# Kernel tuning notes

Hardware: AMD Instinct MI355X
Metric: run time of the kernel (lower is better)

Reference implementation:

```python
import jax, jax.numpy as jnp
import numpy as np

B, T, C = 16, 2048, 68
HEAD = 64

def setup_inputs() -> dict:
    key = jax.random.key(0)
    k1, k2, k3, k4 = jax.random.split(key, 4)
    x = jax.random.normal(k1, (B, T, C), dtype=jnp.float32)
    # Linear(n_embd, head_size, bias=False): y = x @ W, W stored as [C, HEAD]
    Wk = jax.random.normal(k2, (C, HEAD), dtype=jnp.float32) / np.sqrt(C)
    Wq = jax.random.normal(k3, (C, HEAD), dtype=jnp.float32) / np.sqrt(C)
    Wv = jax.random.normal(k4, (C, HEAD), dtype=jnp.float32) / np.sqrt(C)
    return {"x": x, "Wk": Wk, "Wq": Wq, "Wv": Wv}

def reference(x, Wk, Wq, Wv):
    # single-head attention, no causal mask, dropout p=0.0 (identity)
    k = jnp.einsum('btc,ch->bth', x, Wk)   # [B,T,H]
    q = jnp.einsum('btc,ch->bth', x, Wq)   # [B,T,H]
    v = jnp.einsum('btc,ch->bth', x, Wv)   # [B,T,H]
    scale = 1.0 / jnp.sqrt(jnp.asarray(k.shape[-1], k.dtype))
    wei = jnp.einsum('bqh,bkh->bqk', q, k) * scale  # [B,T,T]
    wei = jax.nn.softmax(wei, axis=-1)
    out = jnp.einsum('bqk,bkh->bqh', wei, v)        # [B,T,H]
    return out
```

## Files before the change

kernel.cpp:

```cpp
#include <hip/hip_runtime.h>
#include <hip/hip_bf16.h>

#define BB 16
#define TT 2048
#define CC 68
#define HH 64
#define PP 40

typedef short short8 __attribute__((ext_vector_type(8)));
typedef float floatx4 __attribute__((ext_vector_type(4)));

static __device__ __forceinline__ unsigned short f2bf(float f) {
    union { float f; unsigned u; } v; v.f = f;
    unsigned r = v.u + 0x7fffu + ((v.u >> 16) & 1u);
    return (unsigned short)(r >> 16);
}
static __device__ __forceinline__ unsigned pk2(float a, float b) {
    unsigned ua = __builtin_bit_cast(unsigned, a) + 0x8000u;
    unsigned ub = __builtin_bit_cast(unsigned, b) + 0x8000u;
    return (ua >> 16) | (ub & 0xffff0000u);
}

#define GLD16(gsrc, ldsbase)                                                        \
    __builtin_amdgcn_global_load_lds(                                               \
        (const __attribute__((address_space(1))) unsigned int*)(gsrc),              \
        (__attribute__((address_space(3))) unsigned int*)(ldsbase), 16, 0, 0)

#define WAITV8 asm volatile("s_waitcnt vmcnt(8)" ::: "memory")
#define WAITV0 asm volatile("s_waitcnt vmcnt(0)" ::: "memory")
#define MEMFENCE asm volatile("" ::: "memory")

__global__ __launch_bounds__(256) void prep_w(
        const float* __restrict__ Wk, const float* __restrict__ Wq,
        const float* __restrict__ Wv, unsigned short* __restrict__ Wt) {
    int idx = blockIdx.x * 256 + threadIdx.x;
    if (idx >= 192 * 96) return;
    int n = idx / 96, c = idx - n * 96;
    float v = 0.f;
    if (c < CC) {
        if (n < 64)       v = Wk[c * 64 + n];
        else if (n < 128) v = Wq[c * 64 + (n - 64)] * 0.18033688011112042f;
        else              v = Wv[c * 64 + (n - 128)];
    }
    Wt[idx] = f2bf(v);
}

__global__ __launch_bounds__(256) void qkv_kernel(
        const float* __restrict__ x, const unsigned short* __restrict__ Wt,
        unsigned short* __restrict__ Qb, unsigned short* __restrict__ Kb,
        unsigned short* __restrict__ Vt) {
    int tid = threadIdx.x;
    int wave = tid >> 6, lane = tid & 63, quad = lane >> 4, l15 = lane & 15;
    size_t row0 = (size_t)blockIdx.x * 64;
    int b = (int)(row0 >> 11), t0 = (int)(row0 & 2047);
    size_t myrow = row0 + wave * 16 + l15;
    const float* xr = x + myrow * CC;

    short8 a[3];
    union { short8 s8; unsigned u[4]; } t;
    #pragma unroll
    for (int cs = 0; cs < 2; ++cs) {
        float4 f0 = *(const float4*)(xr + cs * 32 + quad * 8);
        float4 f1 = *(const float4*)(xr + cs * 32 + quad * 8 + 4);
        t.u[0] = pk2(f0.x, f0.y); t.u[1] = pk2(f0.z, f0.w);
        t.u[2] = pk2(f1.x, f1.y); t.u[3] = pk2(f1.z, f1.w);
        a[cs] = t.s8;
    }
    {
        t.u[0] = 0; t.u[1] = 0; t.u[2] = 0; t.u[3] = 0;
        if (quad == 0) {
            float4 f = *(const float4*)(xr + 64);
            t.u[0] = pk2(f.x, f.y); t.u[1] = pk2(f.z, f.w);
        }
        a[2] = t.s8;
    }

    auto loadW = [&](short8 (&w)[3], int nt) {
        #pragma unroll
        for (int cs = 0; cs < 3; ++cs)
            w[cs] = *(const short8*)&Wt[(nt * 16 + l15) * 96 + cs * 32 + quad * 8];
    };

    short8 wf[2][3];
    loadW(wf[0], 0);
    for (int nt = 0; nt < 12; ++nt) {
        if (nt + 1 < 12) loadW(wf[(nt + 1) & 1], nt + 1);
        floatx4 acc = (floatx4){0.f, 0.f, 0.f, 0.f};
        #pragma unroll
        for (int cs = 0; cs < 3; ++cs)
            acc = __builtin_amdgcn_mfma_f32_16x16x32_bf16(a[cs], wf[nt & 1][cs], acc, 0, 0, 0);

        if (nt < 8) {
            unsigned short* dst = (nt < 4) ? Kb : Qb;
            int h = (nt & 3) * 16 + l15;
            #pragma unroll
            for (int r = 0; r < 4; ++r)
                dst[(row0 + wave * 16 + quad * 4 + r) * 64 + h] = f2bf(acc[r]);
        } else {
            int h = (nt - 8) * 16 + l15;
            int tt = t0 + wave * 16 + quad * 4;
            uint2 v2; v2.x = pk2(acc[0], acc[1]); v2.y = pk2(acc[2], acc[3]);
            *(uint2*)&Vt[((size_t)(b * 64 + h)) * TT + tt] = v2;
        }
    }
}

__global__ __launch_bounds__(256) void attn_kernel(
        const unsigned short* __restrict__ Qb,
        const unsigned short* __restrict__ Kb,
        const unsigned short* __restrict__ Vt,
        float* __restrict__ out) {
    __shared__ union {
        unsigned char stg[4][2][8192];
        float accL[64][66];
    } u;
    __shared__ unsigned short Ps[4][32 * PP];
    __shared__ float lL[2][64];

    int tid = threadIdx.x;
    int wave = tid >> 6, lane = tid & 63, quad = lane >> 4, l15 = lane & 15;
    int half = wave >> 1, qh = wave & 1;
    int id = blockIdx.x;
    int b = id & 15, qblk = id >> 4;
    int q0 = qblk * 64 + qh * 32;
    int kbase = half * 1024;
    unsigned short* ps = Ps[wave];

    short8 qf[2][2];
    #pragma unroll
    for (int qs = 0; qs < 2; ++qs)
        #pragma unroll
        for (int kh = 0; kh < 2; ++kh)
            qf[qs][kh] = *(const short8*)&Qb[((size_t)(b * TT + q0 + qs * 16 + l15)) * 64
                                             + kh * 32 + quad * 8];

    floatx4 acc[2][4];
    float lpart[2] = {0.f, 0.f};
    #pragma unroll
    for (int qs = 0; qs < 2; ++qs)
        #pragma unroll
        for (int hb = 0; hb < 4; ++hb) acc[qs][hb] = (floatx4){0.f, 0.f, 0.f, 0.f};

    auto stage = [&](int it, int p) {
        unsigned char* base = u.stg[wave][p];
        int kt = kbase + it * 32;
        #pragma unroll
        for (int i = 0; i < 4; ++i) {
            int ci = i * 64 + lane;
            int kv = ci >> 3, cp = ci & 7, c = cp ^ (kv & 7);
            GLD16(Kb + ((size_t)(b * TT + kt + kv) * 64 + c * 8), base + i * 1024);
        }
        #pragma unroll
        for (int i = 0; i < 4; ++i) {
            int ci = i * 64 + lane;
            int h = ci >> 2, cp = ci & 3, c = cp ^ ((h >> 1) & 3);
            GLD16(Vt + ((size_t)(b * 64 + h) * TT + kt + c * 8), base + 4096 + i * 1024);
        }
    };

    auto compute = [&](int p) {
        const unsigned char* Kbuf = u.stg[wave][p];
        const unsigned char* Vbuf = Kbuf + 4096;

        short8 kf[2][2], vf[4];
        #pragma unroll
        for (int ks = 0; ks < 2; ++ks)
            #pragma unroll
            for (int kh = 0; kh < 2; ++kh) {
                int cp = (kh * 4 + quad) ^ (l15 & 7);
                kf[ks][kh] = *(const short8*)(Kbuf + (ks * 16 + l15) * 128 + cp * 16);
            }
        #pragma unroll
        for (int hb = 0; hb < 4; ++hb) {
            int cp = quad ^ ((l15 >> 1) & 3);
            vf[hb] = *(const short8*)(Vbuf + (hb * 16 + l15) * 64 + cp * 16);
        }

        floatx4 s[2][2];
        #pragma unroll
        for (int qs = 0; qs < 2; ++qs)
            #pragma unroll
            for (int ks = 0; ks < 2; ++ks) {
                floatx4 z = (floatx4){0.f, 0.f, 0.f, 0.f};
                z = __builtin_amdgcn_mfma_f32_16x16x32_bf16(kf[ks][0], qf[qs][0], z, 0, 0, 0);
                z = __builtin_amdgcn_mfma_f32_16x16x32_bf16(kf[ks][1], qf[qs][1], z, 0, 0, 0);
                s[qs][ks] = z;
            }

        #pragma unroll
        for (int qs = 0; qs < 2; ++qs) {
            float lp = 0.f;
            #pragma unroll
            for (int ks = 0; ks < 2; ++ks) {
                float e0 = __builtin_amdgcn_exp2f(s[qs][ks][0]);
                float e1 = __builtin_amdgcn_exp2f(s[qs][ks][1]);
                float e2 = __builtin_amdgcn_exp2f(s[qs][ks][2]);
                float e3 = __builtin_amdgcn_exp2f(s[qs][ks][3]);
                lp += (e0 + e1) + (e2 + e3);
                uint2 w; w.x = pk2(e0, e1); w.y = pk2(e2, e3);
                *(uint2*)&ps[(qs * 16 + l15) * PP + ks * 16 + quad * 4] = w;
            }
            lpart[qs] += lp;
        }

        short8 pf[2];
        #pragma unroll
        for (int qs = 0; qs < 2; ++qs)
            pf[qs] = *(const short8*)&ps[(qs * 16 + l15) * PP + quad * 8];
        #pragma unroll
        for (int qs = 0; qs < 2; ++qs)
            #pragma unroll
            for (int hb = 0; hb < 4; ++hb)
                acc[qs][hb] = __builtin_amdgcn_mfma_f32_16x16x32_bf16(pf[qs], vf[hb], acc[qs][hb], 0, 0, 0);
    };

    stage(0, 0);
    stage(1, 1);
    for (int it = 0; it < 31; ++it) {
        WAITV8;
        compute(it & 1);
        if (it + 2 < 32) { MEMFENCE; stage(it + 2, it & 1); }
    }
    WAITV0;
    compute(1);

    #pragma unroll
    for (int qs = 0; qs < 2; ++qs) {
        float v = lpart[qs];
        v += __shfl_xor(v, 16);
        v += __shfl_xor(v, 32);
        lpart[qs] = v;
    }
    if (quad == 0) {
        lL[half][qh * 32 + l15]      = lpart[0];
        lL[half][qh * 32 + 16 + l15] = lpart[1];
    }
    __syncthreads();

    if (half == 1) {
        #pragma unroll
        for (int qs = 0; qs < 2; ++qs)
            #pragma unroll
            for (int hb = 0; hb < 4; ++hb)
                #pragma unroll
                for (int r = 0; r < 4; ++r)
                    u.accL[qh * 32 + qs * 16 + quad * 4 + r][hb * 16 + l15] = acc[qs][hb][r];
    }
    __syncthreads();

    if (half == 0) {
        #pragma unroll
        for (int qs = 0; qs < 2; ++qs) {
            float rl[4];
            #pragma unroll
            for (int r = 0; r < 4; ++r) {
                int qw = qh * 32 + qs * 16 + quad * 4 + r;
                rl[r] = 1.0f / (lL[0][qw] + lL[1][qw]);
            }
            #pragma unroll
            for (int hb = 0; hb < 4; ++hb)
                #pragma unroll
                for (int r = 0; r < 4; ++r) {
                    int qw = qh * 32 + qs * 16 + quad * 4 + r;
                    float tot = acc[qs][hb][r] + u.accL[qw][hb * 16 + l15];
                    out[((size_t)(b * TT + qblk * 64 + qw)) * 64 + hb * 16 + l15] = tot * rl[r];
                }
        }
    }
}

extern "C" void kernel_launch(void* const* d_in, const int* in_sizes, int n_in,
                              void* d_out, int out_size, void* d_ws, size_t ws_size,
                              hipStream_t stream) {
    const float* x  = (const float*)d_in[0];
    const float* Wk = (const float*)d_in[1];
    const float* Wq = (const float*)d_in[2];
    const float* Wv = (const float*)d_in[3];

    unsigned short* Qb = (unsigned short*)d_ws;
    unsigned short* Kb = Qb + (size_t)BB * TT * HH;
    unsigned short* Vt = Kb + (size_t)BB * TT * HH;
    unsigned short* Wt = Vt + (size_t)BB * TT * HH;
    float* out = (float*)d_out;

    prep_w<<<dim3(72), dim3(256), 0, stream>>>(Wk, Wq, Wv, Wt);
    qkv_kernel<<<dim3(BB * TT / 64), dim3(256), 0, stream>>>(x, Wt, Qb, Kb, Vt);
    attn_kernel<<<dim3(BB * (TT / 64)), dim3(256), 0, stream>>>(Qb, Kb, Vt, out);
}
```

Baseline: 110.0 us.

## Share K/V staging across waves with 512-thread blocks and triple buffering

The attention kernel moves to 512-thread blocks covering 128 queries. Within each key half, one wave loads the K tile and another loads the V tile into a shared triple-buffered LDS stage, where before each wave fetched its own copy. Block barriers now synchronise stage reuse, which cuts redundant global and LDS traffic per query but adds s_barrier stalls and halves the grid to 256 blocks. The qkv kernel also interleaves batches in its block ordering and deepens its weight-fragment prefetch to three buffers.

```diff
diff --git a/kernel.cpp b/kernel.cpp
--- a/kernel.cpp
+++ b/kernel.cpp
@@ -26,9 +26,9 @@
         (const __attribute__((address_space(1))) unsigned int*)(gsrc),              \
         (__attribute__((address_space(3))) unsigned int*)(ldsbase), 16, 0, 0)
 
-#define WAITV8 asm volatile("s_waitcnt vmcnt(8)" ::: "memory")
+#define WAITV4 asm volatile("s_waitcnt vmcnt(4)" ::: "memory")
 #define WAITV0 asm volatile("s_waitcnt vmcnt(0)" ::: "memory")
-#define MEMFENCE asm volatile("" ::: "memory")
+#define BAR    asm volatile("s_barrier" ::: "memory")
 
 __global__ __launch_bounds__(256) void prep_w(
         const float* __restrict__ Wk, const float* __restrict__ Wq,
@@ -51,8 +51,10 @@
         unsigned short* __restrict__ Vt) {
     int tid = threadIdx.x;
     int wave = tid >> 6, lane = tid & 63, quad = lane >> 4, l15 = lane & 15;
-    size_t row0 = (size_t)blockIdx.x * 64;
-    int b = (int)(row0 >> 11), t0 = (int)(row0 & 2047);
+    int id = blockIdx.x;
+    int b = id & 15, rowblk = id >> 4;
+    size_t row0 = (size_t)b * TT + rowblk * 64;
+    int t0 = rowblk * 64;
     size_t myrow = row0 + wave * 16 + l15;
     const float* xr = x + myrow * CC;
 
@@ -81,14 +83,16 @@
             w[cs] = *(const short8*)&Wt[(nt * 16 + l15) * 96 + cs * 32 + quad * 8];
     };
 
-    short8 wf[2][3];
+    short8 wf[3][3];
     loadW(wf[0], 0);
+    loadW(wf[1], 1);
+    #pragma unroll
     for (int nt = 0; nt < 12; ++nt) {
-        if (nt + 1 < 12) loadW(wf[(nt + 1) & 1], nt + 1);
+        if (nt + 2 < 12) loadW(wf[(nt + 2) % 3], nt + 2);
         floatx4 acc = (floatx4){0.f, 0.f, 0.f, 0.f};
         #pragma unroll
         for (int cs = 0; cs < 3; ++cs)
-            acc = __builtin_amdgcn_mfma_f32_16x16x32_bf16(a[cs], wf[nt & 1][cs], acc, 0, 0, 0);
+            acc = __builtin_amdgcn_mfma_f32_16x16x32_bf16(a[cs], wf[nt % 3][cs], acc, 0, 0, 0);
 
         if (nt < 8) {
             unsigned short* dst = (nt < 4) ? Kb : Qb;
@@ -105,24 +109,24 @@
     }
 }
 
-__global__ __launch_bounds__(256) void attn_kernel(
+__global__ __launch_bounds__(512, 2) void attn_kernel(
         const unsigned short* __restrict__ Qb,
         const unsigned short* __restrict__ Kb,
         const unsigned short* __restrict__ Vt,
         float* __restrict__ out) {
     __shared__ union {
-        unsigned char stg[4][2][8192];
-        float accL[64][66];
+        unsigned char stg[2][3][8192];
+        float accL[128][66];
     } u;
-    __shared__ unsigned short Ps[4][32 * PP];
-    __shared__ float lL[2][64];
+    __shared__ unsigned short Ps[8][32 * PP];
+    __shared__ float lL[2][128];
 
     int tid = threadIdx.x;
     int wave = tid >> 6, lane = tid & 63, quad = lane >> 4, l15 = lane & 15;
-    int half = wave >> 1, qh = wave & 1;
+    int half = wave >> 2, qh = wave & 3;
     int id = blockIdx.x;
     int b = id & 15, qblk = id >> 4;
-    int q0 = qblk * 64 + qh * 32;
+    int q0 = qblk * 128 + qh * 32;
     int kbase = half * 1024;
     unsigned short* ps = Ps[wave];
 
@@ -142,24 +146,28 @@
         for (int hb = 0; hb < 4; ++hb) acc[qs][hb] = (floatx4){0.f, 0.f, 0.f, 0.f};
 
     auto stage = [&](int it, int p) {
-        unsigned char* base = u.stg[wave][p];
         int kt = kbase + it * 32;
-        #pragma unroll
-        for (int i = 0; i < 4; ++i) {
-            int ci = i * 64 + lane;
-            int kv = ci >> 3, cp = ci & 7, c = cp ^ (kv & 7);
-            GLD16(Kb + ((size_t)(b * TT + kt + kv) * 64 + c * 8), base + i * 1024);
-        }
-        #pragma unroll
-        for (int i = 0; i < 4; ++i) {
-            int ci = i * 64 + lane;
-            int h = ci >> 2, cp = ci & 3, c = cp ^ ((h >> 1) & 3);
-            GLD16(Vt + ((size_t)(b * 64 + h) * TT + kt + c * 8), base + 4096 + i * 1024);
+        if (qh == 0) {
+            unsigned char* base = u.stg[half][p];
+            #pragma unroll
+            for (int i = 0; i < 4; ++i) {
+                int ci = i * 64 + lane;
+                int kv = ci >> 3, cp = ci & 7, c = cp ^ (kv & 7);
+                GLD16(Kb + ((size_t)(b * TT + kt + kv) * 64 + c * 8), base + i * 1024);
+            }
+        } else if (qh == 1) {
+            unsigned char* base = u.stg[half][p] + 4096;
+            #pragma unroll
+            for (int i = 0; i < 4; ++i) {
+                int ci = i * 64 + lane;
+                int h = ci >> 2, cp = ci & 3, c = cp ^ ((h >> 1) & 3);
+                GLD16(Vt + ((size_t)(b * 64 + h) * TT + kt + c * 8), base + i * 1024);
+            }
         }
     };
 
     auto compute = [&](int p) {
-        const unsigned char* Kbuf = u.stg[wave][p];
+        const unsigned char* Kbuf = u.stg[half][p];
         const unsigned char* Vbuf = Kbuf + 4096;
 
         short8 kf[2][2], vf[4];
@@ -216,13 +224,14 @@
 
     stage(0, 0);
     stage(1, 1);
-    for (int it = 0; it < 31; ++it) {
-        WAITV8;
-        compute(it & 1);
-        if (it + 2 < 32) { MEMFENCE; stage(it + 2, it & 1); }
-    }
-    WAITV0;
-    compute(1);
+    for (int it = 0; it < 32; ++it) {
+        if (qh < 2) {
+            if (it < 31) { WAITV4; } else { WAITV0; }
+        }
+        BAR;
+        if (it + 2 < 32) stage(it + 2, (it + 2) % 3);
+        compute(it % 3);
+    }
 
     #pragma unroll
     for (int qs = 0; qs < 2; ++qs) {
@@ -263,7 +272,7 @@
                 for (int r = 0; r < 4; ++r) {
                     int qw = qh * 32 + qs * 16 + quad * 4 + r;
                     float tot = acc[qs][hb][r] + u.accL[qw][hb * 16 + l15];
-                    out[((size_t)(b * TT + qblk * 64 + qw)) * 64 + hb * 16 + l15] = tot * rl[r];
+                    out[((size_t)(b * TT + qblk * 128 + qw)) * 64 + hb * 16 + l15] = tot * rl[r];
                 }
         }
     }
@@ -285,5 +294,5 @@
 
     prep_w<<<dim3(72), dim3(256), 0, stream>>>(Wk, Wq, Wv, Wt);
     qkv_kernel<<<dim3(BB * TT / 64), dim3(256), 0, stream>>>(x, Wt, Qb, Kb, Vt);
-    attn_kernel<<<dim3(BB * (TT / 64)), dim3(256), 0, stream>>>(Qb, Kb, Vt, out);
-}
+    attn_kernel<<<dim3(BB * (TT / 128)), dim3(512), 0, stream>>>(Qb, Kb, Vt, out);
+}
```

Result: faster. 103.3 us (-6.1%).

## Keep softmax P in registers and split keys four ways across waves

Applied to the files above, without the earlier changes.

The attention kernel now has each wave cover all 64 queries of the block over a quarter of the keys. P stays in registers: the QK^T MFMA output layout is reused directly as the A operand of the PV MFMA, which removes the LDS round trip for P. V fragments are read with permuted 4-element loads so the key ordering matches. The QKV projection is split across twice as many blocks, with operands swapped so K/Q stores become vectorized, and pk2 now rounds to nearest-even. The cost is more accumulator registers per wave and a serialized three-step LDS reduction across waves at the end.

```diff
diff --git a/kernel.cpp b/kernel.cpp
--- a/kernel.cpp
+++ b/kernel.cpp
@@ -5,8 +5,8 @@
 #define TT 2048
 #define CC 68
 #define HH 64
-#define PP 40
-
+
+typedef short bs4 __attribute__((ext_vector_type(4)));
 typedef short short8 __attribute__((ext_vector_type(8)));
 typedef float floatx4 __attribute__((ext_vector_type(4)));
 
@@ -16,8 +16,10 @@
     return (unsigned short)(r >> 16);
 }
 static __device__ __forceinline__ unsigned pk2(float a, float b) {
-    unsigned ua = __builtin_bit_cast(unsigned, a) + 0x8000u;
-    unsigned ub = __builtin_bit_cast(unsigned, b) + 0x8000u;
+    unsigned ua = __builtin_bit_cast(unsigned, a);
+    unsigned ub = __builtin_bit_cast(unsigned, b);
+    ua += 0x7fffu + ((ua >> 16) & 1u);
+    ub += 0x7fffu + ((ub >> 16) & 1u);
     return (ua >> 16) | (ub & 0xffff0000u);
 }
 
@@ -51,12 +53,14 @@
         unsigned short* __restrict__ Vt) {
     int tid = threadIdx.x;
     int wave = tid >> 6, lane = tid & 63, quad = lane >> 4, l15 = lane & 15;
-    size_t row0 = (size_t)blockIdx.x * 64;
-    int b = (int)(row0 >> 11), t0 = (int)(row0 & 2047);
-    size_t myrow = row0 + wave * 16 + l15;
-    const float* xr = x + myrow * CC;
-
-    short8 a[3];
+    int id = blockIdx.x;
+    int b = id & 15, rowblk = id >> 4;
+    int t0 = rowblk * 32 + (wave & 1) * 16;
+    int nt0 = (wave >> 1) * 6;
+    size_t row0 = (size_t)b * TT + t0;
+
+    const float* xr = x + (row0 + l15) * CC;
+    short8 xf[3];
     union { short8 s8; unsigned u[4]; } t;
     #pragma unroll
     for (int cs = 0; cs < 2; ++cs) {
@@ -64,7 +68,7 @@
         float4 f1 = *(const float4*)(xr + cs * 32 + quad * 8 + 4);
         t.u[0] = pk2(f0.x, f0.y); t.u[1] = pk2(f0.z, f0.w);
         t.u[2] = pk2(f1.x, f1.y); t.u[3] = pk2(f1.z, f1.w);
-        a[cs] = t.s8;
+        xf[cs] = t.s8;
     }
     {
         t.u[0] = 0; t.u[1] = 0; t.u[2] = 0; t.u[3] = 0;
@@ -72,35 +76,34 @@
             float4 f = *(const float4*)(xr + 64);
             t.u[0] = pk2(f.x, f.y); t.u[1] = pk2(f.z, f.w);
         }
-        a[2] = t.s8;
-    }
-
-    auto loadW = [&](short8 (&w)[3], int nt) {
+        xf[2] = t.s8;
+    }
+
+    short8 wf[6][3];
+    #pragma unroll
+    for (int nt = 0; nt < 6; ++nt)
         #pragma unroll
         for (int cs = 0; cs < 3; ++cs)
-            w[cs] = *(const short8*)&Wt[(nt * 16 + l15) * 96 + cs * 32 + quad * 8];
-    };
-
-    short8 wf[2][3];
-    loadW(wf[0], 0);
-    for (int nt = 0; nt < 12; ++nt) {
-        if (nt + 1 < 12) loadW(wf[(nt + 1) & 1], nt + 1);
+            wf[nt][cs] = *(const short8*)&Wt[((nt0 + nt) * 16 + l15) * 96 + cs * 32 + quad * 8];
+
+    #pragma unroll
+    for (int nt = 0; nt < 6; ++nt) {
+        int gn = nt0 + nt;
         floatx4 acc = (floatx4){0.f, 0.f, 0.f, 0.f};
         #pragma unroll
         for (int cs = 0; cs < 3; ++cs)
-            acc = __builtin_amdgcn_mfma_f32_16x16x32_bf16(a[cs], wf[nt & 1][cs], acc, 0, 0, 0);
-
-        if (nt < 8) {
-            unsigned short* dst = (nt < 4) ? Kb : Qb;
-            int h = (nt & 3) * 16 + l15;
+            acc = __builtin_amdgcn_mfma_f32_16x16x32_bf16(wf[nt][cs], xf[cs], acc, 0, 0, 0);
+
+        if (gn < 8) {
+            unsigned short* dst = (gn < 4) ? Kb : Qb;
+            int h0 = (gn & 3) * 16 + quad * 4;
+            uint2 v2; v2.x = pk2(acc[0], acc[1]); v2.y = pk2(acc[2], acc[3]);
+            *(uint2*)&dst[(row0 + l15) * 64 + h0] = v2;
+        } else {
+            int h0 = (gn - 8) * 16 + quad * 4;
             #pragma unroll
             for (int r = 0; r < 4; ++r)
-                dst[(row0 + wave * 16 + quad * 4 + r) * 64 + h] = f2bf(acc[r]);
-        } else {
-            int h = (nt - 8) * 16 + l15;
-            int tt = t0 + wave * 16 + quad * 4;
-            uint2 v2; v2.x = pk2(acc[0], acc[1]); v2.y = pk2(acc[2], acc[3]);
-            *(uint2*)&Vt[((size_t)(b * 64 + h)) * TT + tt] = v2;
+                Vt[((size_t)(b * 64 + h0 + r)) * TT + t0 + l15] = f2bf(acc[r]);
         }
     }
 }
@@ -114,30 +117,27 @@
         unsigned char stg[4][2][8192];
         float accL[64][66];
     } u;
-    __shared__ unsigned short Ps[4][32 * PP];
-    __shared__ float lL[2][64];
+    __shared__ float lL[4][64];
 
     int tid = threadIdx.x;
     int wave = tid >> 6, lane = tid & 63, quad = lane >> 4, l15 = lane & 15;
-    int half = wave >> 1, qh = wave & 1;
     int id = blockIdx.x;
     int b = id & 15, qblk = id >> 4;
-    int q0 = qblk * 64 + qh * 32;
-    int kbase = half * 1024;
-    unsigned short* ps = Ps[wave];
-
-    short8 qf[2][2];
-    #pragma unroll
-    for (int qs = 0; qs < 2; ++qs)
+    int q0 = qblk * 64;
+    int kbase = wave * 512;
+
+    short8 qf[4][2];
+    #pragma unroll
+    for (int qs = 0; qs < 4; ++qs)
         #pragma unroll
         for (int kh = 0; kh < 2; ++kh)
             qf[qs][kh] = *(const short8*)&Qb[((size_t)(b * TT + q0 + qs * 16 + l15)) * 64
                                              + kh * 32 + quad * 8];
 
-    floatx4 acc[2][4];
-    float lpart[2] = {0.f, 0.f};
-    #pragma unroll
-    for (int qs = 0; qs < 2; ++qs)
+    floatx4 acc[4][4];
+    float lpart[4] = {0.f, 0.f, 0.f, 0.f};
+    #pragma unroll
+    for (int qs = 0; qs < 4; ++qs)
         #pragma unroll
         for (int hb = 0; hb < 4; ++hb) acc[qs][hb] = (floatx4){0.f, 0.f, 0.f, 0.f};
 
@@ -145,40 +145,49 @@
         unsigned char* base = u.stg[wave][p];
         int kt = kbase + it * 32;
         #pragma unroll
-        for (int i = 0; i < 4; ++i) {
-            int ci = i * 64 + lane;
-            int kv = ci >> 3, cp = ci & 7, c = cp ^ (kv & 7);
-            GLD16(Kb + ((size_t)(b * TT + kt + kv) * 64 + c * 8), base + i * 1024);
-        }
-        #pragma unroll
-        for (int i = 0; i < 4; ++i) {
-            int ci = i * 64 + lane;
-            int h = ci >> 2, cp = ci & 3, c = cp ^ ((h >> 1) & 3);
-            GLD16(Vt + ((size_t)(b * 64 + h) * TT + kt + c * 8), base + 4096 + i * 1024);
+        for (int i2 = 0; i2 < 4; ++i2) {
+            int ci = i2 * 64 + lane;
+            int kv = ci >> 3, c = (ci & 7) ^ (kv & 7);
+            GLD16(Kb + ((size_t)(b * TT + kt + kv) * 64 + c * 8), base + i2 * 1024);
+        }
+        #pragma unroll
+        for (int i2 = 0; i2 < 4; ++i2) {
+            int ci = i2 * 64 + lane;
+            int h = ci >> 2, blkk = (ci & 3) ^ ((h >> 1) & 3);
+            GLD16(Vt + ((size_t)(b * 64 + h) * TT + kt + blkk * 8), base + 4096 + i2 * 1024);
         }
     };
 
-    auto compute = [&](int p) {
+    stage(0, 0);
+    stage(1, 1);
+
+    for (int it = 0; it < 16; ++it) {
+        if (it < 15) { WAITV8; } else { WAITV0; }
+        int p = it & 1;
         const unsigned char* Kbuf = u.stg[wave][p];
         const unsigned char* Vbuf = Kbuf + 4096;
 
-        short8 kf[2][2], vf[4];
+        short8 kf[2][2];
         #pragma unroll
         for (int ks = 0; ks < 2; ++ks)
             #pragma unroll
             for (int kh = 0; kh < 2; ++kh) {
-                int cp = (kh * 4 + quad) ^ (l15 & 7);
-                kf[ks][kh] = *(const short8*)(Kbuf + (ks * 16 + l15) * 128 + cp * 16);
+                int kvr = ks * 16 + l15;
+                kf[ks][kh] = *(const short8*)(Kbuf + kvr * 128
+                                              + (((kh * 4 + quad) ^ (kvr & 7)) * 16));
             }
+        union { short8 s8; bs4 s4[2]; } vf[4];
         #pragma unroll
         for (int hb = 0; hb < 4; ++hb) {
-            int cp = quad ^ ((l15 >> 1) & 3);
-            vf[hb] = *(const short8*)(Vbuf + (hb * 16 + l15) * 64 + cp * 16);
-        }
-
-        floatx4 s[2][2];
-        #pragma unroll
-        for (int qs = 0; qs < 2; ++qs)
+            int h = hb * 16 + l15;
+            int a0 = h * 64 + ((quad ^ (h & 6)) * 8);
+            vf[hb].s4[0] = *(const bs4*)(Vbuf + a0);
+            vf[hb].s4[1] = *(const bs4*)(Vbuf + (a0 ^ 32));
+        }
+
+        floatx4 s[4][2];
+        #pragma unroll
+        for (int qs = 0; qs < 4; ++qs)
             #pragma unroll
             for (int ks = 0; ks < 2; ++ks) {
                 floatx4 z = (floatx4){0.f, 0.f, 0.f, 0.f};
@@ -188,82 +197,87 @@
             }
 
         #pragma unroll
-        for (int qs = 0; qs < 2; ++qs) {
-            float lp = 0.f;
-            #pragma unroll
-            for (int ks = 0; ks < 2; ++ks) {
-                float e0 = __builtin_amdgcn_exp2f(s[qs][ks][0]);
-                float e1 = __builtin_amdgcn_exp2f(s[qs][ks][1]);
-                float e2 = __builtin_amdgcn_exp2f(s[qs][ks][2]);
-                float e3 = __builtin_amdgcn_exp2f(s[qs][ks][3]);
-                lp += (e0 + e1) + (e2 + e3);
-                uint2 w; w.x = pk2(e0, e1); w.y = pk2(e2, e3);
-                *(uint2*)&ps[(qs * 16 + l15) * PP + ks * 16 + quad * 4] = w;
-            }
-            lpart[qs] += lp;
-        }
-
-        short8 pf[2];
-        #pragma unroll
-        for (int qs = 0; qs < 2; ++qs)
-            pf[qs] = *(const short8*)&ps[(qs * 16 + l15) * PP + quad * 8];
-        #pragma unroll
-        for (int qs = 0; qs < 2; ++qs)
-            #pragma unroll
-            for (int hb = 0; hb < 4; ++hb)
-                acc[qs][hb] = __builtin_amdgcn_mfma_f32_16x16x32_bf16(pf[qs], vf[hb], acc[qs][hb], 0, 0, 0);
-    };
-
-    stage(0, 0);
-    stage(1, 1);
-    for (int it = 0; it < 31; ++it) {
-        WAITV8;
-        compute(it & 1);
-        if (it + 2 < 32) { MEMFENCE; stage(it + 2, it & 1); }
-    }
-    WAITV0;
-    compute(1);
-
-    #pragma unroll
-    for (int qs = 0; qs < 2; ++qs) {
+        for (int qs = 0; qs < 4; ++qs) {
+            float e0 = __builtin_amdgcn_exp2f(s[qs][0][0]);
+            float e1 = __builtin_amdgcn_exp2f(s[qs][0][1]);
+            float e2 = __builtin_amdgcn_exp2f(s[qs][0][2]);
+            float e3 = __builtin_amdgcn_exp2f(s[qs][0][3]);
+            float e4 = __builtin_amdgcn_exp2f(s[qs][1][0]);
+            float e5 = __builtin_amdgcn_exp2f(s[qs][1][1]);
+            float e6 = __builtin_amdgcn_exp2f(s[qs][1][2]);
+            float e7 = __builtin_amdgcn_exp2f(s[qs][1][3]);
+            lpart[qs] += ((e0 + e1) + (e2 + e3)) + ((e4 + e5) + (e6 + e7));
+            union { short8 s8; unsigned u[4]; } pw;
+            pw.u[0] = pk2(e0, e1); pw.u[1] = pk2(e2, e3);
+            pw.u[2] = pk2(e4, e5); pw.u[3] = pk2(e6, e7);
+            #pragma unroll
+            for (int hb = 0; hb < 4; ++hb)
+                acc[qs][hb] = __builtin_amdgcn_mfma_f32_16x16x32_bf16(pw.s8, vf[hb].s8, acc[qs][hb], 0, 0, 0);
+        }
+
+        MEMFENCE;
+        if (it + 2 < 16) stage(it + 2, p);
+    }
+
+    #pragma unroll
+    for (int qs = 0; qs < 4; ++qs) {
         float v = lpart[qs];
         v += __shfl_xor(v, 16);
         v += __shfl_xor(v, 32);
         lpart[qs] = v;
     }
     if (quad == 0) {
-        lL[half][qh * 32 + l15]      = lpart[0];
-        lL[half][qh * 32 + 16 + l15] = lpart[1];
+        #pragma unroll
+        for (int qs = 0; qs < 4; ++qs) lL[wave][qs * 16 + l15] = lpart[qs];
     }
     __syncthreads();
 
-    if (half == 1) {
-        #pragma unroll
-        for (int qs = 0; qs < 2; ++qs)
+    if (wave == 3) {
+        #pragma unroll
+        for (int qs = 0; qs < 4; ++qs)
             #pragma unroll
             for (int hb = 0; hb < 4; ++hb)
                 #pragma unroll
                 for (int r = 0; r < 4; ++r)
-                    u.accL[qh * 32 + qs * 16 + quad * 4 + r][hb * 16 + l15] = acc[qs][hb][r];
+                    u.accL[qs * 16 + quad * 4 + r][hb * 16 + l15] = acc[qs][hb][r];
     }
     __syncthreads();
-
-    if (half == 0) {
-        #pragma unroll
-        for (int qs = 0; qs < 2; ++qs) {
+    if (wave == 2) {
+        #pragma unroll
+        for (int qs = 0; qs < 4; ++qs)
+            #pragma unroll
+            for (int hb = 0; hb < 4; ++hb)
+                #pragma unroll
+                for (int r = 0; r < 4; ++r)
+                    u.accL[qs * 16 + quad * 4 + r][hb * 16 + l15] += acc[qs][hb][r];
+    }
+    __syncthreads();
+    if (wave == 1) {
+        #pragma unroll
+        for (int qs = 0; qs < 4; ++qs)
+            #pragma unroll
+            for (int hb = 0; hb < 4; ++hb)
+                #pragma unroll
+                for (int r = 0; r < 4; ++r)
+                    u.accL[qs * 16 + quad * 4 + r][hb * 16 + l15] += acc[qs][hb][r];
+    }
+    __syncthreads();
+    if (wave == 0) {
+        #pragma unroll
+        for (int qs = 0; qs < 4; ++qs) {
             float rl[4];
             #pragma unroll
             for (int r = 0; r < 4; ++r) {
-                int qw = qh * 32 + qs * 16 + quad * 4 + r;
-                rl[r] = 1.0f / (lL[0][qw] + lL[1][qw]);
+                int ql = qs * 16 + quad * 4 + r;
+                rl[r] = 1.0f / (((lL[0][ql] + lL[1][ql]) + (lL[2][ql] + lL[3][ql])));
             }
             #pragma unroll
             for (int hb = 0; hb < 4; ++hb)
                 #pragma unroll
                 for (int r = 0; r < 4; ++r) {
-                    int qw = qh * 32 + qs * 16 + quad * 4 + r;
-                    float tot = acc[qs][hb][r] + u.accL[qw][hb * 16 + l15];
-                    out[((size_t)(b * TT + qblk * 64 + qw)) * 64 + hb * 16 + l15] = tot * rl[r];
+                    int ql = qs * 16 + quad * 4 + r;
+                    float tot = acc[qs][hb][r] + u.accL[ql][hb * 16 + l15];
+                    out[((size_t)(b * TT + q0 + ql)) * 64 + hb * 16 + l15] = tot * rl[r];
                 }
         }
     }
@@ -284,6 +298,6 @@
     float* out = (float*)d_out;
 
     prep_w<<<dim3(72), dim3(256), 0, stream>>>(Wk, Wq, Wv, Wt);
-    qkv_kernel<<<dim3(BB * TT / 64), dim3(256), 0, stream>>>(x, Wt, Qb, Kb, Vt);
+    qkv_kernel<<<dim3(2 * BB * TT / 64), dim3(256), 0, stream>>>(x, Wt, Qb, Kb, Vt);
     attn_kernel<<<dim3(BB * (TT / 64)), dim3(256), 0, stream>>>(Qb, Kb, Vt, out);
 }
```

After: 111.1 us. No clear change (+1.0%).
